# Optimization experiments

Hardware: AMD Instinct MI355X
Metric: run time of the kernel (lower is better)

The kernel has to match this reference:

```python
import jax, jax.numpy as jnp
import numpy as np

NX, NQ, NU, NY = 256, 64, 8, 4
N = 65536
EPS = 0.01
STD = 0.5


def setup_inputs() -> dict:
    key = jax.random.key(0)
    ks = jax.random.split(key, 8)
    return {
        "x": jax.random.normal(ks[0], (N, NX), jnp.float32),
        "u": jax.random.normal(ks[1], (N, NU), jnp.float32),
        "X": jax.random.normal(ks[2], (NX + NQ, NX + NQ), jnp.float32) * STD,
        "U": jax.random.normal(ks[3], (NX, NQ), jnp.float32) * STD,
        "Y1": jax.random.normal(ks[4], (NX, NX), jnp.float32) * STD,
        "XP": jax.random.normal(ks[5], (NX, NX), jnp.float32) * STD,
        "B2": jax.random.normal(ks[6], (NX, NU), jnp.float32) * STD,
        "D12": jax.random.normal(ks[7], (NQ, NU), jnp.float32) * STD,
        "bv": jnp.zeros((NQ,), jnp.float32),
        "t": 0,
    }


def _constrained(X, U, Y1, XP):
    # updateParameters(): build A, B1, C1, D11 from unconstrained params.
    P = XP @ XP.T + EPS * jnp.eye(NX, dtype=XP.dtype)
    H = X @ X.T + EPS * jnp.eye(NX + NQ, dtype=X.dtype)
    H11, H12, H22 = H[:NX, :NX], H[:NX, NX:], H[NX:, NX:]
    Y = -0.5 * (H11 + Y1 - Y1.T)
    Pinv = jnp.linalg.inv(P)
    A = Pinv @ Y                                   # [nx, nx]
    lam = 0.5 * jnp.diagonal(H22)                  # Lambda diagonal
    D11 = -jnp.tril(H22, -1) / lam[:, None]        # strictly lower triangular [nq, nq]
    C1 = U.T / lam[:, None]                        # [nq, nx]
    B1 = Pinv @ (-H12 - U)                         # [nx, nq]
    return A, B1, C1, D11


def _calc_w(base, D11):
    # Forward substitution: w_i = relu(base_i + sum_{j<i} D11[i,j] * w_j).
    # D11 is strictly lower triangular and unfilled w columns are zero, so a
    # full matvec against the carry is exact.
    nq = base.shape[1]

    def step(w, inp):
        i, row, b_col = inp                        # row: [nq], b_col: [Nbatch]
        wi = jax.nn.relu(b_col + w @ row)
        return w.at[:, i].set(wi), None

    w0 = jnp.zeros_like(base)
    w, _ = jax.lax.scan(step, w0, (jnp.arange(nq), D11, base.T))
    return w


def reference(x, u, X, U, Y1, XP, B2, D12, bv, t):
    A, B1, C1, D11 = _constrained(X, U, Y1, XP)
    base = x @ C1.T + u @ D12.T + bv               # [N, nq]
    w = _calc_w(base, D11)
    x_dot = x @ A.T + w @ B1.T + u @ B2.T          # [N, nx]
    return x_dot
```

## Files before the change

### kernel.cpp

```cpp
#include <hip/hip_runtime.h>

#define EPS_C 0.01f

typedef __attribute__((ext_vector_type(8))) short short8;
typedef __attribute__((ext_vector_type(4))) float f32x4;
typedef __attribute__((ext_vector_type(4))) unsigned short u16x4;
typedef __attribute__((ext_vector_type(8))) unsigned short u16x8;

#define WS_H    0
#define WS_C    102400
#define WS_C2   167936
#define WS_Y    233472
#define WS_RHS  299008
#define WS_D11  331776
#define WS_WFH  419840
#define WS_WFM  464896
#define WS_WFL  509952
#define WS_BBH  555008
#define WS_BBM  564224
#define WS_BBL  573440
#define WS_WG   582656
#define WS_E0   4776960
#define WS_E1   4781056

__device__ __forceinline__ int wfoff(int n, int k) {
    return (((n >> 4) * 44 + (k >> 5) * 4 + ((k >> 3) & 3)) << 7) + ((n & 15) << 3) + (k & 7);
}
__device__ __forceinline__ int bboff(int n, int k) {
    return (((n >> 4) * 36 + (k >> 5) * 4 + ((k >> 3) & 3)) << 7) + ((n & 15) << 3) + (k & 7);
}

__device__ __forceinline__ unsigned short f2bf(float f) {
    unsigned int u = __float_as_uint(f);
    unsigned int r = (u + 0x7fffu + ((u >> 16) & 1u)) >> 16;
    return (unsigned short)r;
}
__device__ __forceinline__ float bf2f(unsigned short h) {
    return __uint_as_float(((unsigned int)h) << 16);
}
__device__ __forceinline__ void split1(float f, unsigned short& h, unsigned short& m, unsigned short& l) {
    h = f2bf(f);
    float r1 = f - bf2f(h);
    m = f2bf(r1);
    l = f2bf(r1 - bf2f(m));
}
__device__ __forceinline__ void split8(const float* v, short8& h8, short8& m8, short8& l8) {
#pragma unroll
    for (int j = 0; j < 8; ++j) {
        unsigned short h, m, l;
        split1(v[j], h, m, l);
        h8[j] = (short)h; m8[j] = (short)m; l8[j] = (short)l;
    }
}

__global__ void k_build(const float* __restrict__ Xm, const float* __restrict__ XPm,
                        float* __restrict__ H, float* __restrict__ P) {
    int idx = blockIdx.x * 256 + threadIdx.x;
    if (idx < 102400) {
        int i = idx / 320, j = idx - i * 320;
        const float4* a = (const float4*)(Xm + i * 320);
        const float4* b = (const float4*)(Xm + j * 320);
        float s = 0.f;
        for (int k = 0; k < 80; ++k) {
            float4 va = a[k], vb = b[k];
            s += va.x * vb.x + va.y * vb.y + va.z * vb.z + va.w * vb.w;
        }
        H[idx] = (i == j) ? s + EPS_C : s;
    } else {
        idx -= 102400;
        if (idx < 65536) {
            int i = idx >> 8, j = idx & 255;
            const float4* a = (const float4*)(XPm + i * 256);
            const float4* b = (const float4*)(XPm + j * 256);
            float s = 0.f;
            for (int k = 0; k < 64; ++k) {
                float4 va = a[k], vb = b[k];
                s += va.x * vb.x + va.y * vb.y + va.z * vb.z + va.w * vb.w;
            }
            P[idx] = (i == j) ? s + EPS_C : s;
        }
    }
}

__global__ void k_derived(const float* __restrict__ H, const float* __restrict__ Um,
                          const float* __restrict__ Y1, const float* __restrict__ B2,
                          const float* __restrict__ D12,
                          float* __restrict__ Y, float* __restrict__ RHS,
                          float* __restrict__ D11g,
                          unsigned short* __restrict__ Bh, unsigned short* __restrict__ Bm,
                          unsigned short* __restrict__ Bl,
                          unsigned short* __restrict__ Bbh, unsigned short* __restrict__ Bbm,
                          unsigned short* __restrict__ Bbl) {
    int idx = blockIdx.x * 256 + threadIdx.x;
    if (idx < 65536) {
        int i = idx >> 8, j = idx & 255;
        Y[idx] = -0.5f * (H[i * 320 + j] + Y1[i * 256 + j] - Y1[j * 256 + i]);
        return;
    }
    idx -= 65536;
    if (idx < 16384) {
        RHS[idx] = -H[(idx >> 6) * 320 + 256 + (idx & 63)] - Um[idx];
        return;
    }
    idx -= 16384;
    if (idx < 4096) {
        int q = idx >> 6, j = idx & 63;
        float lam = 0.5f * H[(256 + q) * 320 + 256 + q];
        D11g[idx] = (j < q) ? -H[(256 + q) * 320 + 256 + j] / lam : 0.f;
        return;
    }
    idx -= 4096;
    if (idx < 8192) {
        int o = idx >> 5, cc = idx & 31;
        float f = (cc < 8) ? B2[o * 8 + cc] : 0.f;
        unsigned short h, m, l;
        split1(f, h, m, l);
        int off = wfoff(o, 256 + cc);
        Bh[off] = h; Bm[off] = m; Bl[off] = l;
        return;
    }
    idx -= 8192;
    if (idx < 18432) {
        int q = idx / 288, k = idx - q * 288;
        float f;
        if (k < 256) {
            float lam = 0.5f * H[(256 + q) * 320 + 256 + q];
            f = Um[(size_t)k * 64 + q] / lam;
        } else if (k < 264) f = D12[(size_t)q * 8 + (k - 256)];
        else f = 0.f;
        unsigned short h, m, l;
        split1(f, h, m, l);
        int off = bboff(q, k);
        Bbh[off] = h; Bbm[off] = m; Bbl[off] = l;
    }
}

__global__ void __launch_bounds__(256) k_inv8(const float* __restrict__ Cold, float* __restrict__ E, int b) {
    __shared__ __align__(16) float M[64 * 68];
    __shared__ __align__(16) float Rs[8 * 68];
    __shared__ __align__(16) float Ts[64 * 8];
    __shared__ float E8s[8 * 9];
    const int tid = threadIdx.x;
    const int ti = tid & 15, tj = tid >> 4;
#pragma unroll
    for (int t = 0; t < 4; ++t) {
        int e = tid + t * 256;
        int r = e >> 4, c4 = e & 15;
        float4 v = *(const float4*)&Cold[(size_t)(b * 64 + r) * 256 + b * 64 + c4 * 4];
        *(float4*)&M[r * 68 + c4 * 4] = v;
    }
    __syncthreads();
    for (int s = 0; s < 8; ++s) {
        if (tid < 64) {
            const int lane = tid;
            float e8[8];
#pragma unroll
            for (int j = 0; j < 8; ++j) e8[j] = 0.f;
            if (lane < 8) {
#pragma unroll
                for (int j = 0; j < 8; ++j) e8[j] = M[(s * 8 + lane) * 68 + s * 8 + j];
            }
#pragma unroll
            for (int k = 0; k < 8; ++k) {
                const float p = __shfl(e8[k], k);
                const float rinv = 1.0f / p;
                const float f = -e8[k] * rinv;
                const bool isk = (lane == k);
#pragma unroll
                for (int j = 0; j < 8; ++j) {
                    const float prj = __shfl(e8[j], k);
                    if (j == k) e8[j] = isk ? rinv : f;
                    else        e8[j] = isk ? prj * rinv : fmaf(f, prj, e8[j]);
                }
            }
            if (lane < 8) {
#pragma unroll
                for (int j = 0; j < 8; ++j) E8s[lane * 9 + j] = e8[j];
            }
        }
        __syncthreads();
#pragma unroll
        for (int t = 0; t < 2; ++t) {
            int e = tid + t * 256;
            int r = e >> 6, c = e & 63;
            Rs[r * 68 + c] = M[(s * 8 + r) * 68 + c];
        }
#pragma unroll
        for (int t = 0; t < 2; ++t) {
            int e = tid + t * 256;
            int i = e >> 3, c = e & 7;
            float acc = 0.f;
#pragma unroll
            for (int j = 0; j < 8; ++j) acc = fmaf(M[i * 68 + s * 8 + j], E8s[j * 9 + c], acc);
            Ts[i * 8 + c] = acc;
        }
        __syncthreads();
        {
            const bool rowIn = ((ti >> 1) == s);
            const bool colIn = ((tj >> 1) == s);
            const int i0 = ti * 4, j0 = tj * 4;
            float nv[4][4];
            if (rowIn && colIn) {
#pragma unroll
                for (int r = 0; r < 4; ++r)
#pragma unroll
                    for (int d = 0; d < 4; ++d)
                        nv[r][d] = E8s[(i0 - s * 8 + r) * 9 + (j0 - s * 8 + d)];
            } else if (rowIn) {
#pragma unroll
                for (int r = 0; r < 4; ++r)
#pragma unroll
                    for (int d = 0; d < 4; ++d) {
                        float acc = 0.f;
#pragma unroll
                        for (int c = 0; c < 8; ++c)
                            acc = fmaf(E8s[(i0 - s * 8 + r) * 9 + c], Rs[c * 68 + j0 + d], acc);
                        nv[r][d] = acc;
                    }
            } else if (colIn) {
#pragma unroll
                for (int r = 0; r < 4; ++r)
#pragma unroll
                    for (int d = 0; d < 4; ++d)
                        nv[r][d] = -Ts[(i0 + r) * 8 + (j0 - s * 8 + d)];
            } else {
#pragma unroll
                for (int r = 0; r < 4; ++r)
#pragma unroll
                    for (int d = 0; d < 4; ++d) {
                        float acc = M[(i0 + r) * 68 + j0 + d];
#pragma unroll
                        for (int c = 0; c < 8; ++c)
                            acc = fmaf(-Ts[(i0 + r) * 8 + c], Rs[c * 68 + j0 + d], acc);
                        nv[r][d] = acc;
                    }
            }
#pragma unroll
            for (int r = 0; r < 4; ++r)
#pragma unroll
                for (int d = 0; d < 4; ++d) M[(i0 + r) * 68 + j0 + d] = nv[r][d];
        }
        __syncthreads();
    }
#pragma unroll
    for (int t = 0; t < 4; ++t) {
        int e = tid + t * 256;
        int r = e >> 4, c4 = e & 15;
        float4 v = *(const float4*)&M[r * 68 + c4 * 4];
        *(float4*)&E[(size_t)r * 64 + c4 * 4] = v;
    }
}

__global__ void __launch_bounds__(256) k_gjS(const float* __restrict__ Cold, float* __restrict__ Cnew,
                                             const float* __restrict__ E, float* __restrict__ Eout,
                                             int b, int nb) {
    const int I = blockIdx.x >> 2, J = blockIdx.x & 3;
    const int tid = threadIdx.x;
    const int ti = tid & 15, tj = tid >> 4;
    if (I == b && J == b) {
        const int r = tid >> 2, seg = tid & 3;
#pragma unroll
        for (int t = 0; t < 4; ++t) {
            float4 v = *(const float4*)&E[(size_t)r * 64 + seg * 16 + t * 4];
            *(float4*)&Cnew[(size_t)(b * 64 + r) * 256 + b * 64 + seg * 16 + t * 4] = v;
        }
        return;
    }
    __shared__ __align__(16) float Es[64 * 68];
    __shared__ __align__(16) float S1[64 * 68];
    __shared__ __align__(16) float S2[64 * 68];
    for (int e = tid; e < 1024; e += 256) {
        int r = e >> 4, c4 = e & 15;
        float4 v = *(const float4*)&E[(size_t)r * 64 + c4 * 4];
        *(float4*)&Es[r * 68 + c4 * 4] = v;
    }
    if (I == b) {
        for (int e = tid; e < 1024; e += 256) {
            int r = e >> 4, c4 = e & 15;
            float4 v = *(const float4*)&Cold[(size_t)(b * 64 + r) * 256 + J * 64 + c4 * 4];
            *(float4*)&S1[r * 68 + c4 * 4] = v;
        }
        __syncthreads();
        float acc[4][4];
#pragma unroll
        for (int r = 0; r < 4; ++r)
#pragma unroll
            for (int d = 0; d < 4; ++d) acc[r][d] = 0.f;
        for (int mm = 0; mm < 64; ++mm) {
            float a4[4], b4[4];
#pragma unroll
            for (int d = 0; d < 4; ++d) { a4[d] = Es[(ti * 4 + d) * 68 + mm]; b4[d] = S1[mm * 68 + tj * 4 + d]; }
#pragma unroll
            for (int r = 0; r < 4; ++r)
#pragma unroll
                for (int d = 0; d < 4; ++d) acc[r][d] = fmaf(a4[r], b4[d], acc[r][d]);
        }
#pragma unroll
        for (int r = 0; r < 4; ++r) {
            float4 v = {acc[r][0], acc[r][1], acc[r][2], acc[r][3]};
            *(float4*)&Cnew[(size_t)(b * 64 + ti * 4 + r) * 256 + J * 64 + tj * 4] = v;
        }
        return;
    }
    if (J == b) {
        for (int e = tid; e < 1024; e += 256) {
            int r = e >> 4, c4 = e & 15;
            float4 v = *(const float4*)&Cold[(size_t)(I * 64 + r) * 256 + b * 64 + c4 * 4];
            *(float4*)&S1[r * 68 + c4 * 4] = v;
        }
        __syncthreads();
        float acc[4][4];
#pragma unroll
        for (int r = 0; r < 4; ++r)
#pragma unroll
            for (int d = 0; d < 4; ++d) acc[r][d] = 0.f;
        for (int kk = 0; kk < 64; ++kk) {
            float a4[4], b4[4];
#pragma unroll
            for (int d = 0; d < 4; ++d) { a4[d] = S1[(ti * 4 + d) * 68 + kk]; b4[d] = Es[kk * 68 + tj * 4 + d]; }
#pragma unroll
            for (int r = 0; r < 4; ++r)
#pragma unroll
                for (int d = 0; d < 4; ++d) acc[r][d] = fmaf(a4[r], b4[d], acc[r][d]);
        }
#pragma unroll
        for (int r = 0; r < 4; ++r) {
            float4 v = {-acc[r][0], -acc[r][1], -acc[r][2], -acc[r][3]};
            *(float4*)&Cnew[(size_t)(I * 64 + ti * 4 + r) * 256 + b * 64 + tj * 4] = v;
        }
        return;
    }
    for (int e = tid; e < 1024; e += 256) {
        int r = e >> 4, c4 = e & 15;
        float4 v = *(const float4*)&Cold[(size_t)(I * 64 + r) * 256 + b * 64 + c4 * 4];
        *(float4*)&S1[r * 68 + c4 * 4] = v;
        float4 w = *(const float4*)&Cold[(size_t)(b * 64 + r) * 256 + J * 64 + c4 * 4];
        *(float4*)&S2[r * 68 + c4 * 4] = w;
    }
    __syncthreads();
    float t4[4][4];
#pragma unroll
    for (int r = 0; r < 4; ++r)
#pragma unroll
        for (int d = 0; d < 4; ++d) t4[r][d] = 0.f;
    for (int kk = 0; kk < 64; ++kk) {
        float a4[4], b4[4];
#pragma unroll
        for (int d = 0; d < 4; ++d) { a4[d] = S1[(ti * 4 + d) * 68 + kk]; b4[d] = Es[kk * 68 + tj * 4 + d]; }
#pragma unroll
        for (int r = 0; r < 4; ++r)
#pragma unroll
            for (int d = 0; d < 4; ++d) t4[r][d] = fmaf(a4[r], b4[d], t4[r][d]);
    }
    __syncthreads();
#pragma unroll
    for (int r = 0; r < 4; ++r)
#pragma unroll
        for (int d = 0; d < 4; ++d) S1[(ti * 4 + r) * 68 + tj * 4 + d] = t4[r][d];
    __syncthreads();
    float acc[4][4];
#pragma unroll
    for (int r = 0; r < 4; ++r) {
        float4 cv = *(const float4*)&Cold[(size_t)(I * 64 + ti * 4 + r) * 256 + J * 64 + tj * 4];
        acc[r][0] = cv.x; acc[r][1] = cv.y; acc[r][2] = cv.z; acc[r][3] = cv.w;
    }
    for (int kk = 0; kk < 64; ++kk) {
        float a4[4], b4[4];
#pragma unroll
        for (int d = 0; d < 4; ++d) { a4[d] = S1[(ti * 4 + d) * 68 + kk]; b4[d] = S2[kk * 68 + tj * 4 + d]; }
#pragma unroll
        for (int r = 0; r < 4; ++r)
#pragma unroll
            for (int d = 0; d < 4; ++d) acc[r][d] = fmaf(-a4[r], b4[d], acc[r][d]);
    }
#pragma unroll
    for (int r = 0; r < 4; ++r) {
        float4 v = {acc[r][0], acc[r][1], acc[r][2], acc[r][3]};
        *(float4*)&Cnew[(size_t)(I * 64 + ti * 4 + r) * 256 + J * 64 + tj * 4] = v;
    }
    if (I == nb && J == nb) {
        float* M   = Es;
        float* Rs2 = S2;
        float* Ts2 = S2 + 1024;
        float* E8s = S2 + 1664;
        __syncthreads();
#pragma unroll
        for (int r = 0; r < 4; ++r)
#pragma unroll
            for (int d = 0; d < 4; ++d)
                M[(ti * 4 + r) * 68 + tj * 4 + d] = acc[r][d];
        __syncthreads();
        for (int s = 0; s < 8; ++s) {
            if (tid < 64) {
                const int lane = tid;
                float e8[8];
#pragma unroll
                for (int j = 0; j < 8; ++j) e8[j] = 0.f;
                if (lane < 8) {
#pragma unroll
                    for (int j = 0; j < 8; ++j) e8[j] = M[(s * 8 + lane) * 68 + s * 8 + j];
                }
#pragma unroll
                for (int k = 0; k < 8; ++k) {
                    const float p = __shfl(e8[k], k);
                    const float rinv = 1.0f / p;
                    const float f = -e8[k] * rinv;
                    const bool isk = (lane == k);
#pragma unroll
                    for (int j = 0; j < 8; ++j) {
                        const float prj = __shfl(e8[j], k);
                        if (j == k) e8[j] = isk ? rinv : f;
                        else        e8[j] = isk ? prj * rinv : fmaf(f, prj, e8[j]);
                    }
                }
                if (lane < 8) {
#pragma unroll
                    for (int j = 0; j < 8; ++j) E8s[lane * 9 + j] = e8[j];
                }
            }
            __syncthreads();
#pragma unroll
            for (int t = 0; t < 2; ++t) {
                int e = tid + t * 256;
                int r = e >> 6, c = e & 63;
                Rs2[r * 68 + c] = M[(s * 8 + r) * 68 + c];
            }
#pragma unroll
            for (int t = 0; t < 2; ++t) {
                int e = tid + t * 256;
                int i = e >> 3, c = e & 7;
                float a2 = 0.f;
#pragma unroll
                for (int j = 0; j < 8; ++j) a2 = fmaf(M[i * 68 + s * 8 + j], E8s[j * 9 + c], a2);
                Ts2[i * 8 + c] = a2;
            }
            __syncthreads();
            {
                const bool rowIn = ((ti >> 1) == s);
                const bool colIn = ((tj >> 1) == s);
                const int i0 = ti * 4, j0 = tj * 4;
                float nv[4][4];
                if (rowIn && colIn) {
#pragma unroll
                    for (int r = 0; r < 4; ++r)
#pragma unroll
                        for (int d = 0; d < 4; ++d)
                            nv[r][d] = E8s[(i0 - s * 8 + r) * 9 + (j0 - s * 8 + d)];
                } else if (rowIn) {
#pragma unroll
                    for (int r = 0; r < 4; ++r)
#pragma unroll
                        for (int d = 0; d < 4; ++d) {
                            float a2 = 0.f;
#pragma unroll
                            for (int c = 0; c < 8; ++c)
                                a2 = fmaf(E8s[(i0 - s * 8 + r) * 9 + c], Rs2[c * 68 + j0 + d], a2);
                            nv[r][d] = a2;
                        }
                } else if (colIn) {
#pragma unroll
                    for (int r = 0; r < 4; ++r)
#pragma unroll
                        for (int d = 0; d < 4; ++d)
                            nv[r][d] = -Ts2[(i0 + r) * 8 + (j0 - s * 8 + d)];
                } else {
#pragma unroll
                    for (int r = 0; r < 4; ++r)
#pragma unroll
                        for (int d = 0; d < 4; ++d) {
                            float a2 = M[(i0 + r) * 68 + j0 + d];
#pragma unroll
                            for (int c = 0; c < 8; ++c)
                                a2 = fmaf(-Ts2[(i0 + r) * 8 + c], Rs2[c * 68 + j0 + d], a2);
                            nv[r][d] = a2;
                        }
                }
#pragma unroll
                for (int r = 0; r < 4; ++r)
#pragma unroll
                    for (int d = 0; d < 4; ++d) M[(i0 + r) * 68 + j0 + d] = nv[r][d];
            }
            __syncthreads();
        }
#pragma unroll
        for (int t = 0; t < 4; ++t) {
            int e = tid + t * 256;
            int r = e >> 4, c4 = e & 15;
            float4 v = *(const float4*)&M[r * 68 + c4 * 4];
            *(float4*)&Eout[(size_t)r * 64 + c4 * 4] = v;
        }
    }
}

__global__ void __launch_bounds__(256) k_apply2(const float* __restrict__ PI, const float* __restrict__ Y,
                                                const float* __restrict__ RHS,
                                                unsigned short* __restrict__ Bh, unsigned short* __restrict__ Bm,
                                                unsigned short* __restrict__ Bl) {
    const int i0 = ((int)blockIdx.x / 5) * 64;
    const int c0 = ((int)blockIdx.x % 5) * 64;
    __shared__ __align__(16) float S1[64 * 68], S2[64 * 68];
    const int tid = threadIdx.x;
    const int ti = tid & 15, tj = tid >> 4;
    float acc[4][4];
#pragma unroll
    for (int r = 0; r < 4; ++r)
#pragma unroll
        for (int d = 0; d < 4; ++d) acc[r][d] = 0.f;
    for (int kc = 0; kc < 4; ++kc) {
        __syncthreads();
        for (int e = tid; e < 1024; e += 256) {
            int i = e >> 4, k4 = e & 15;
            float4 v = *(const float4*)&PI[(size_t)(i0 + i) * 256 + kc * 64 + k4 * 4];
            S1[(k4 * 4 + 0) * 68 + i] = v.x;
            S1[(k4 * 4 + 1) * 68 + i] = v.y;
            S1[(k4 * 4 + 2) * 68 + i] = v.z;
            S1[(k4 * 4 + 3) * 68 + i] = v.w;
            float4 w;
            if (c0 < 256) w = *(const float4*)&Y[(size_t)(kc * 64 + i) * 256 + c0 + k4 * 4];
            else          w = *(const float4*)&RHS[(size_t)(kc * 64 + i) * 64 + k4 * 4];
            *(float4*)&S2[i * 68 + k4 * 4] = w;
        }
        __syncthreads();
        for (int kk = 0; kk < 64; ++kk) {
            float4 pv = *(const float4*)&S1[kk * 68 + ti * 4];
            float4 gv = *(const float4*)&S2[kk * 68 + tj * 4];
            float p4[4] = {pv.x, pv.y, pv.z, pv.w};
            float g4[4] = {gv.x, gv.y, gv.z, gv.w};
#pragma unroll
            for (int r = 0; r < 4; ++r)
#pragma unroll
                for (int d = 0; d < 4; ++d) acc[r][d] = fmaf(p4[r], g4[d], acc[r][d]);
        }
    }
    const int pc0 = (c0 < 256) ? c0 : 288;
#pragma unroll
    for (int r = 0; r < 4; ++r)
#pragma unroll
        for (int d = 0; d < 4; ++d) {
            unsigned short h, m, l;
            split1(acc[r][d], h, m, l);
            int off = wfoff(i0 + ti * 4 + r, pc0 + tj * 4 + d);
            Bh[off] = h; Bm[off] = m; Bl[off] = l;
        }
}

#define XSTR 264
__global__ void __launch_bounds__(256, 3) k_base(const float* __restrict__ x, const float* __restrict__ u,
                                                 const unsigned short* __restrict__ Bbh,
                                                 const unsigned short* __restrict__ Bbm,
                                                 const unsigned short* __restrict__ Bbl,
                                                 const float* __restrict__ bv,
                                                 float* __restrict__ wg) {
    __shared__ __align__(16) unsigned short Ah[32 * XSTR];
    __shared__ __align__(16) unsigned short Am[32 * XSTR];
    __shared__ __align__(16) unsigned short Al[32 * XSTR];
    const int tid = threadIdx.x;
    const int r0 = blockIdx.x * 32;
    {
        const float4* xg4 = (const float4*)(x + (size_t)r0 * 256);
#pragma unroll
        for (int i = 0; i < 8; ++i) {
            int e = tid + i * 256, r = e >> 6, c4 = e & 63;
            float4 v = xg4[e];
            float vv[4] = {v.x, v.y, v.z, v.w};
            u16x4 hv, mv, lv;
#pragma unroll
            for (int j = 0; j < 4; ++j) {
                unsigned short h, m, l;
                split1(vv[j], h, m, l);
                hv[j] = h; mv[j] = m; lv[j] = l;
            }
            *(u16x4*)&Ah[r * XSTR + c4 * 4] = hv;
            *(u16x4*)&Am[r * XSTR + c4 * 4] = mv;
            *(u16x4*)&Al[r * XSTR + c4 * 4] = lv;
        }
    }
    __syncthreads();
    const int lane = tid & 63, wid = tid >> 6;
    const int n0 = wid * 16;
    const int lr = lane & 15, lg = lane >> 4;
    const int lk = lg * 8;
    const int fb = wid * 4608 + lg * 128 + lr * 8;
    f32x4 acc[2];
    acc[0] = (f32x4){0.f, 0.f, 0.f, 0.f};
    acc[1] = (f32x4){0.f, 0.f, 0.f, 0.f};
    for (int kt = 0; kt < 9; ++kt) {
        const int ka = kt * 32 + lk;
        short8 a_h[2], a_m[2], a_l[2];
        if (kt < 8) {
            a_h[0] = *(const short8*)&Ah[lr * XSTR + ka];
            a_h[1] = *(const short8*)&Ah[(16 + lr) * XSTR + ka];
            a_m[0] = *(const short8*)&Am[lr * XSTR + ka];
            a_m[1] = *(const short8*)&Am[(16 + lr) * XSTR + ka];
            a_l[0] = *(const short8*)&Al[lr * XSTR + ka];
            a_l[1] = *(const short8*)&Al[(16 + lr) * XSTR + ka];
        } else {
            if (lg == 0) {
                float vv[8];
                const float4* up = (const float4*)&u[(size_t)(r0 + lr) * 8];
                float4 v0 = up[0], v1 = up[1];
                vv[0] = v0.x; vv[1] = v0.y; vv[2] = v0.z; vv[3] = v0.w;
                vv[4] = v1.x; vv[5] = v1.y; vv[6] = v1.z; vv[7] = v1.w;
                split8(vv, a_h[0], a_m[0], a_l[0]);
                const float4* up2 = (const float4*)&u[(size_t)(r0 + 16 + lr) * 8];
                float4 w0 = up2[0], w1 = up2[1];
                vv[0] = w0.x; vv[1] = w0.y; vv[2] = w0.z; vv[3] = w0.w;
                vv[4] = w1.x; vv[5] = w1.y; vv[6] = w1.z; vv[7] = w1.w;
                split8(vv, a_h[1], a_m[1], a_l[1]);
            } else {
                short8 z = {0, 0, 0, 0, 0, 0, 0, 0};
                a_h[0] = z; a_h[1] = z; a_m[0] = z; a_m[1] = z; a_l[0] = z; a_l[1] = z;
            }
        }
        const int off = fb + kt * 512;
        short8 b_h = *(const short8*)&Bbh[off];
        short8 b_m = *(const short8*)&Bbm[off];
        short8 b_l = *(const short8*)&Bbl[off];
#pragma unroll
        for (int m = 0; m < 2; ++m) {
            acc[m] = __builtin_amdgcn_mfma_f32_16x16x32_bf16(a_h[m], b_h, acc[m], 0, 0, 0);
            acc[m] = __builtin_amdgcn_mfma_f32_16x16x32_bf16(a_m[m], b_h, acc[m], 0, 0, 0);
            acc[m] = __builtin_amdgcn_mfma_f32_16x16x32_bf16(a_h[m], b_m, acc[m], 0, 0, 0);
            acc[m] = __builtin_amdgcn_mfma_f32_16x16x32_bf16(a_l[m], b_h, acc[m], 0, 0, 0);
            acc[m] = __builtin_amdgcn_mfma_f32_16x16x32_bf16(a_m[m], b_m, acc[m], 0, 0, 0);
            acc[m] = __builtin_amdgcn_mfma_f32_16x16x32_bf16(a_h[m], b_l, acc[m], 0, 0, 0);
        }
    }
    const float bvv = bv[n0 + lr];
#pragma unroll
    for (int m = 0; m < 2; ++m)
#pragma unroll
        for (int j = 0; j < 4; ++j)
            wg[(size_t)(r0 + m * 16 + lg * 4 + j) * 64 + n0 + lr] = acc[m][j] + bvv;
}

__global__ void __launch_bounds__(256) k_rec(float* __restrict__ wg, const float* __restrict__ D11g) {
    __shared__ float D[64 * 64];
    const int tid = threadIdx.x;
#pragma unroll
    for (int t = 0; t < 16; ++t) D[tid + t * 256] = D11g[tid + t * 256];
    __syncthreads();
    const size_t r = (size_t)blockIdx.x * 256 + tid;
    float w[64];
    float* wr = wg + r * 64;
#pragma unroll
    for (int c = 0; c < 16; ++c) {
        float4 v = *(const float4*)&wr[c * 4];
        w[4 * c] = v.x; w[4 * c + 1] = v.y; w[4 * c + 2] = v.z; w[4 * c + 3] = v.w;
    }
    w[0] = fmaxf(w[0], 0.f);
#pragma unroll
    for (int i = 1; i < 64; ++i) {
        float s0 = w[i], s1 = 0.f, s2 = 0.f, s3 = 0.f;
#pragma unroll
        for (int j = 0; j + 3 < i; j += 4) {
            s0 = fmaf(w[j + 0], D[i * 64 + j + 0], s0);
            s1 = fmaf(w[j + 1], D[i * 64 + j + 1], s1);
            s2 = fmaf(w[j + 2], D[i * 64 + j + 2], s2);
            s3 = fmaf(w[j + 3], D[i * 64 + j + 3], s3);
        }
#pragma unroll
        for (int j = i & ~3; j < i; ++j) s0 = fmaf(w[j], D[i * 64 + j], s0);
        w[i] = fmaxf((s0 + s1) + (s2 + s3), 0.f);
    }
#pragma unroll
    for (int c = 0; c < 16; ++c) {
        float4 v = {w[4 * c], w[4 * c + 1], w[4 * c + 2], w[4 * c + 3]};
        *(float4*)&wr[c * 4] = v;
    }
}

__global__ void __launch_bounds__(256, 3) k_m2(const float* __restrict__ x, const float* __restrict__ wg,
                                               const float* __restrict__ u,
                                               const unsigned short* __restrict__ Bh,
                                               const unsigned short* __restrict__ Bm,
                                               const unsigned short* __restrict__ Bl,
                                               float* __restrict__ out) {
    __shared__ __align__(16) unsigned short Ah[32 * XSTR];
    __shared__ __align__(16) unsigned short Am[32 * XSTR];
    __shared__ __align__(16) unsigned short Al[32 * XSTR];
    const int tid = threadIdx.x;
    const int r0 = blockIdx.x * 32;
    {
        const float4* xg4 = (const float4*)(x + (size_t)r0 * 256);
#pragma unroll
        for (int i = 0; i < 8; ++i) {
            int e = tid + i * 256, r = e >> 6, c4 = e & 63;
            float4 v = xg4[e];
            float vv[4] = {v.x, v.y, v.z, v.w};
            u16x4 hv, mv, lv;
#pragma unroll
            for (int j = 0; j < 4; ++j) {
                unsigned short h, m, l;
                split1(vv[j], h, m, l);
                hv[j] = h; mv[j] = m; lv[j] = l;
            }
            *(u16x4*)&Ah[r * XSTR + c4 * 4] = hv;
            *(u16x4*)&Am[r * XSTR + c4 * 4] = mv;
            *(u16x4*)&Al[r * XSTR + c4 * 4] = lv;
        }
    }
    __syncthreads();
    const int lane = tid & 63, wid = tid >> 6;
    const int n0 = wid * 64;
    const int lr = lane & 15, lg = lane >> 4;
    const int lk = lg * 8;
    const int lgoff = lg * 128 + lr * 8;
    int fb[4];
#pragma unroll
    for (int nf = 0; nf < 4; ++nf) fb[nf] = (wid * 4 + nf) * 5632 + lgoff;
    f32x4 acc[2][4];
#pragma unroll
    for (int m = 0; m < 2; ++m)
#pragma unroll
        for (int nf = 0; nf < 4; ++nf) acc[m][nf] = (f32x4){0.f, 0.f, 0.f, 0.f};

#define M2_MFMA6()                                                                               \
    for (int nf = 0; nf < 4; ++nf) {                                                             \
        for (int m = 0; m < 2; ++m) {                                                            \
            acc[m][nf] = __builtin_amdgcn_mfma_f32_16x16x32_bf16(a_h[m], b_h[nf], acc[m][nf], 0, 0, 0); \
            acc[m][nf] = __builtin_amdgcn_mfma_f32_16x16x32_bf16(a_m[m], b_h[nf], acc[m][nf], 0, 0, 0); \
            acc[m][nf] = __builtin_amdgcn_mfma_f32_16x16x32_bf16(a_h[m], b_m[nf], acc[m][nf], 0, 0, 0); \
            acc[m][nf] = __builtin_amdgcn_mfma_f32_16x16x32_bf16(a_l[m], b_h[nf], acc[m][nf], 0, 0, 0); \
            acc[m][nf] = __builtin_amdgcn_mfma_f32_16x16x32_bf16(a_m[m], b_m[nf], acc[m][nf], 0, 0, 0); \
            acc[m][nf] = __builtin_amdgcn_mfma_f32_16x16x32_bf16(a_h[m], b_l[nf], acc[m][nf], 0, 0, 0); \
        }                                                                                        \
    }

    for (int kt = 0; kt < 8; ++kt) {
        const int ka = kt * 32 + lk;
        short8 a_h[2], a_m[2], a_l[2];
        a_h[0] = *(const short8*)&Ah[lr * XSTR + ka];
        a_h[1] = *(const short8*)&Ah[(16 + lr) * XSTR + ka];
        a_m[0] = *(const short8*)&Am[lr * XSTR + ka];
        a_m[1] = *(const short8*)&Am[(16 + lr) * XSTR + ka];
        a_l[0] = *(const short8*)&Al[lr * XSTR + ka];
        a_l[1] = *(const short8*)&Al[(16 + lr) * XSTR + ka];
        short8 b_h[4], b_m[4], b_l[4];
#pragma unroll
        for (int nf = 0; nf < 4; ++nf) {
            const int off = fb[nf] + kt * 512;
            b_h[nf] = *(const short8*)&Bh[off];
            b_m[nf] = *(const short8*)&Bm[off];
            b_l[nf] = *(const short8*)&Bl[off];
        }
#pragma unroll
        M2_MFMA6()
    }
    {
        short8 a_h[2], a_m[2], a_l[2];
        if (lg == 0) {
            float vv[8];
            const float4* up = (const float4*)&u[(size_t)(r0 + lr) * 8];
            float4 v0 = up[0], v1 = up[1];
            vv[0] = v0.x; vv[1] = v0.y; vv[2] = v0.z; vv[3] = v0.w;
            vv[4] = v1.x; vv[5] = v1.y; vv[6] = v1.z; vv[7] = v1.w;
            split8(vv, a_h[0], a_m[0], a_l[0]);
            const float4* up2 = (const float4*)&u[(size_t)(r0 + 16 + lr) * 8];
            float4 w0 = up2[0], w1 = up2[1];
            vv[0] = w0.x; vv[1] = w0.y; vv[2] = w0.z; vv[3] = w0.w;
            vv[4] = w1.x; vv[5] = w1.y; vv[6] = w1.z; vv[7] = w1.w;
            split8(vv, a_h[1], a_m[1], a_l[1]);
        } else {
            short8 z = {0, 0, 0, 0, 0, 0, 0, 0};
            a_h[0] = z; a_h[1] = z; a_m[0] = z; a_m[1] = z; a_l[0] = z; a_l[1] = z;
        }
        short8 b_h[4], b_m[4], b_l[4];
#pragma unroll
        for (int nf = 0; nf < 4; ++nf) {
            const int off = fb[nf] + 8 * 512;
            b_h[nf] = *(const short8*)&Bh[off];
            b_m[nf] = *(const short8*)&Bm[off];
            b_l[nf] = *(const short8*)&Bl[off];
        }
#pragma unroll
        M2_MFMA6()
    }
    for (int kt = 9; kt < 11; ++kt) {
        const int wc = (kt - 9) * 32 + lk;
        short8 a_h[2], a_m[2], a_l[2];
        {
            float vv[8];
            const float4* wp = (const float4*)&wg[(size_t)(r0 + lr) * 64 + wc];
            float4 v0 = wp[0], v1 = wp[1];
            vv[0] = v0.x; vv[1] = v0.y; vv[2] = v0.z; vv[3] = v0.w;
            vv[4] = v1.x; vv[5] = v1.y; vv[6] = v1.z; vv[7] = v1.w;
            split8(vv, a_h[0], a_m[0], a_l[0]);
            const float4* wp2 = (const float4*)&wg[(size_t)(r0 + 16 + lr) * 64 + wc];
            float4 w0 = wp2[0], w1 = wp2[1];
            vv[0] = w0.x; vv[1] = w0.y; vv[2] = w0.z; vv[3] = w0.w;
            vv[4] = w1.x; vv[5] = w1.y; vv[6] = w1.z; vv[7] = w1.w;
            split8(vv, a_h[1], a_m[1], a_l[1]);
        }
        short8 b_h[4], b_m[4], b_l[4];
#pragma unroll
        for (int nf = 0; nf < 4; ++nf) {
            const int off = fb[nf] + kt * 512;
            b_h[nf] = *(const short8*)&Bh[off];
            b_m[nf] = *(const short8*)&Bm[off];
            b_l[nf] = *(const short8*)&Bl[off];
        }
#pragma unroll
        for (int nf = 0; nf < 4; ++nf) {
#pragma unroll
            for (int m = 0; m < 2; ++m) {
                acc[m][nf] = __builtin_amdgcn_mfma_f32_16x16x32_bf16(a_h[m], b_h[nf], acc[m][nf], 0, 0, 0);
                acc[m][nf] = __builtin_amdgcn_mfma_f32_16x16x32_bf16(a_m[m], b_h[nf], acc[m][nf], 0, 0, 0);
                acc[m][nf] = __builtin_amdgcn_mfma_f32_16x16x32_bf16(a_h[m], b_m[nf], acc[m][nf], 0, 0, 0);
                acc[m][nf] = __builtin_amdgcn_mfma_f32_16x16x32_bf16(a_l[m], b_h[nf], acc[m][nf], 0, 0, 0);
                acc[m][nf] = __builtin_amdgcn_mfma_f32_16x16x32_bf16(a_m[m], b_m[nf], acc[m][nf], 0, 0, 0);
                acc[m][nf] = __builtin_amdgcn_mfma_f32_16x16x32_bf16(a_h[m], b_l[nf], acc[m][nf], 0, 0, 0);
                acc[m][nf] = __builtin_amdgcn_mfma_f32_16x16x32_bf16(a_m[m], b_l[nf], acc[m][nf], 0, 0, 0);
                acc[m][nf] = __builtin_amdgcn_mfma_f32_16x16x32_bf16(a_l[m], b_m[nf], acc[m][nf], 0, 0, 0);
            }
        }
    }
#pragma unroll
    for (int m = 0; m < 2; ++m)
#pragma unroll
        for (int nf = 0; nf < 4; ++nf)
#pragma unroll
            for (int j = 0; j < 4; ++j)
                out[(size_t)(r0 + m * 16 + lg * 4 + j) * 256 + n0 + nf * 16 + lr] = acc[m][nf][j];
}

extern "C" void kernel_launch(void* const* d_in, const int* in_sizes, int n_in,
                              void* d_out, int out_size, void* d_ws, size_t ws_size,
                              hipStream_t stream) {
    const float* x   = (const float*)d_in[0];
    const float* u   = (const float*)d_in[1];
    const float* Xm  = (const float*)d_in[2];
    const float* Um  = (const float*)d_in[3];
    const float* Y1  = (const float*)d_in[4];
    const float* XPm = (const float*)d_in[5];
    const float* B2  = (const float*)d_in[6];
    const float* D12 = (const float*)d_in[7];
    const float* bv  = (const float*)d_in[8];
    float* out = (float*)d_out;
    float* ws  = (float*)d_ws;

    float* H    = ws + WS_H;
    float* C0   = ws + WS_C;
    float* C1   = ws + WS_C2;
    float* Y    = ws + WS_Y;
    float* RHS  = ws + WS_RHS;
    float* D11g = ws + WS_D11;
    float* E0   = ws + WS_E0;
    float* E1   = ws + WS_E1;
    unsigned short* Bh  = (unsigned short*)(ws + WS_WFH);
    unsigned short* Bm  = (unsigned short*)(ws + WS_WFM);
    unsigned short* Bl  = (unsigned short*)(ws + WS_WFL);
    unsigned short* Bbh = (unsigned short*)(ws + WS_BBH);
    unsigned short* Bbm = (unsigned short*)(ws + WS_BBM);
    unsigned short* Bbl = (unsigned short*)(ws + WS_BBL);
    float* wg = ws + WS_WG;

    k_build<<<656, 256, 0, stream>>>(Xm, XPm, H, C0);
    k_derived<<<441, 256, 0, stream>>>(H, Um, Y1, B2, D12, Y, RHS, D11g,
                                       Bh, Bm, Bl, Bbh, Bbm, Bbl);
    k_base<<<2048, 256, 0, stream>>>(x, u, Bbh, Bbm, Bbl, bv, wg);
    k_rec<<<256, 256, 0, stream>>>(wg, D11g);
    k_inv8<<<1, 256, 0, stream>>>(C0, E0, 0);
    k_gjS<<<16, 256, 0, stream>>>(C0, C1, E0, E1, 0, 1);
    k_gjS<<<16, 256, 0, stream>>>(C1, C0, E1, E0, 1, 2);
    k_gjS<<<16, 256, 0, stream>>>(C0, C1, E0, E1, 2, 3);
    k_gjS<<<16, 256, 0, stream>>>(C1, C0, E1, E0, 3, -1);
    k_apply2<<<20, 256, 0, stream>>>(C0, Y, RHS, Bh, Bm, Bl);
    k_m2<<<2048, 256, 0, stream>>>(x, wg, u, Bh, Bm, Bl, out);
}
```

Before: 340.7 us.

## Fuse recurrence into base GEMM and merge first block inverse into derived kernel

```diff
diff --git a/kernel.cpp b/kernel.cpp
--- a/kernel.cpp
+++ b/kernel.cpp
@@ -82,7 +82,7 @@
     }
 }
 
-__global__ void k_derived(const float* __restrict__ H, const float* __restrict__ Um,
+__global__ void __launch_bounds__(256) k_derived(const float* __restrict__ H, const float* __restrict__ Um,
                           const float* __restrict__ Y1, const float* __restrict__ B2,
                           const float* __restrict__ D12,
                           float* __restrict__ Y, float* __restrict__ RHS,
@@ -90,8 +90,125 @@
                           unsigned short* __restrict__ Bh, unsigned short* __restrict__ Bm,
                           unsigned short* __restrict__ Bl,
                           unsigned short* __restrict__ Bbh, unsigned short* __restrict__ Bbm,
-                          unsigned short* __restrict__ Bbl) {
-    int idx = blockIdx.x * 256 + threadIdx.x;
+                          unsigned short* __restrict__ Bbl,
+                          const float* __restrict__ C0, float* __restrict__ E0) {
+    __shared__ __align__(16) float M[64 * 68];
+    __shared__ __align__(16) float Rs[8 * 68];
+    __shared__ __align__(16) float Ts[64 * 8];
+    __shared__ float E8s[8 * 9];
+    const int tid = threadIdx.x;
+    if (blockIdx.x == 441) {
+        const int ti = tid & 15, tj = tid >> 4;
+#pragma unroll
+        for (int t = 0; t < 4; ++t) {
+            int e = tid + t * 256;
+            int r = e >> 4, c4 = e & 15;
+            float4 v = *(const float4*)&C0[(size_t)r * 256 + c4 * 4];
+            *(float4*)&M[r * 68 + c4 * 4] = v;
+        }
+        __syncthreads();
+        for (int s = 0; s < 8; ++s) {
+            if (tid < 64) {
+                const int lane = tid;
+                float e8[8];
+#pragma unroll
+                for (int j = 0; j < 8; ++j) e8[j] = 0.f;
+                if (lane < 8) {
+#pragma unroll
+                    for (int j = 0; j < 8; ++j) e8[j] = M[(s * 8 + lane) * 68 + s * 8 + j];
+                }
+#pragma unroll
+                for (int k = 0; k < 8; ++k) {
+                    const float p = __shfl(e8[k], k);
+                    const float rinv = 1.0f / p;
+                    const float f = -e8[k] * rinv;
+                    const bool isk = (lane == k);
+#pragma unroll
+                    for (int j = 0; j < 8; ++j) {
+                        const float prj = __shfl(e8[j], k);
+                        if (j == k) e8[j] = isk ? rinv : f;
+                        else        e8[j] = isk ? prj * rinv : fmaf(f, prj, e8[j]);
+                    }
+                }
+                if (lane < 8) {
+#pragma unroll
+                    for (int j = 0; j < 8; ++j) E8s[lane * 9 + j] = e8[j];
+                }
+            }
+            __syncthreads();
+#pragma unroll
+            for (int t = 0; t < 2; ++t) {
+                int e = tid + t * 256;
+                int r = e >> 6, c = e & 63;
+                Rs[r * 68 + c] = M[(s * 8 + r) * 68 + c];
+            }
+#pragma unroll
+            for (int t = 0; t < 2; ++t) {
+                int e = tid + t * 256;
+                int i = e >> 3, c = e & 7;
+                float acc = 0.f;
+#pragma unroll
+                for (int j = 0; j < 8; ++j) acc = fmaf(M[i * 68 + s * 8 + j], E8s[j * 9 + c], acc);
+                Ts[i * 8 + c] = acc;
+            }
+            __syncthreads();
+            {
+                const bool rowIn = ((ti >> 1) == s);
+                const bool colIn = ((tj >> 1) == s);
+                const int i0 = ti * 4, j0 = tj * 4;
+                float nv[4][4];
+                if (rowIn && colIn) {
+#pragma unroll
+                    for (int r = 0; r < 4; ++r)
+#pragma unroll
+                        for (int d = 0; d < 4; ++d)
+                            nv[r][d] = E8s[(i0 - s * 8 + r) * 9 + (j0 - s * 8 + d)];
+                } else if (rowIn) {
+#pragma unroll
+                    for (int r = 0; r < 4; ++r)
+#pragma unroll
+                        for (int d = 0; d < 4; ++d) {
+                            float acc = 0.f;
+#pragma unroll
+                            for (int c = 0; c < 8; ++c)
+                                acc = fmaf(E8s[(i0 - s * 8 + r) * 9 + c], Rs[c * 68 + j0 + d], acc);
+                            nv[r][d] = acc;
+                        }
+                } else if (colIn) {
+#pragma unroll
+                    for (int r = 0; r < 4; ++r)
+#pragma unroll
+                        for (int d = 0; d < 4; ++d)
+                            nv[r][d] = -Ts[(i0 + r) * 8 + (j0 - s * 8 + d)];
+                } else {
+#pragma unroll
+                    for (int r = 0; r < 4; ++r)
+#pragma unroll
+                        for (int d = 0; d < 4; ++d) {
+                            float acc = M[(i0 + r) * 68 + j0 + d];
+#pragma unroll
+                            for (int c = 0; c < 8; ++c)
+                                acc = fmaf(-Ts[(i0 + r) * 8 + c], Rs[c * 68 + j0 + d], acc);
+                            nv[r][d] = acc;
+                        }
+                }
+#pragma unroll
+                for (int r = 0; r < 4; ++r)
+#pragma unroll
+                    for (int d = 0; d < 4; ++d) M[(i0 + r) * 68 + j0 + d] = nv[r][d];
+            }
+            __syncthreads();
+        }
+#pragma unroll
+        for (int t = 0; t < 4; ++t) {
+            int e = tid + t * 256;
+            int r = e >> 4, c4 = e & 15;
+            float4 v = *(const float4*)&M[r * 68 + c4 * 4];
+            *(float4*)&E0[(size_t)r * 64 + c4 * 4] = v;
+        }
+        return;
+    }
+    int idx = blockIdx.x * 256 + tid;
     if (idx < 65536) {
         int i = idx >> 8, j = idx & 255;
         Y[idx] = -0.5f * (H[i * 320 + j] + Y1[i * 256 + j] - Y1[j * 256 + i]);
@@ -132,122 +249,6 @@
         split1(f, h, m, l);
         int off = bboff(q, k);
         Bbh[off] = h; Bbm[off] = m; Bbl[off] = l;
-    }
-}
-
-__global__ void __launch_bounds__(256) k_inv8(const float* __restrict__ Cold, float* __restrict__ E, int b) {
-    __shared__ __align__(16) float M[64 * 68];
-    __shared__ __align__(16) float Rs[8 * 68];
-    __shared__ __align__(16) float Ts[64 * 8];
-    __shared__ float E8s[8 * 9];
-    const int tid = threadIdx.x;
-    const int ti = tid & 15, tj = tid >> 4;
-#pragma unroll
-    for (int t = 0; t < 4; ++t) {
-        int e = tid + t * 256;
-        int r = e >> 4, c4 = e & 15;
-        float4 v = *(const float4*)&Cold[(size_t)(b * 64 + r) * 256 + b * 64 + c4 * 4];
-        *(float4*)&M[r * 68 + c4 * 4] = v;
-    }
-    __syncthreads();
-    for (int s = 0; s < 8; ++s) {
-        if (tid < 64) {
-            const int lane = tid;
-            float e8[8];
-#pragma unroll
-            for (int j = 0; j < 8; ++j) e8[j] = 0.f;
-            if (lane < 8) {
-#pragma unroll
-                for (int j = 0; j < 8; ++j) e8[j] = M[(s * 8 + lane) * 68 + s * 8 + j];
-            }
-#pragma unroll
-            for (int k = 0; k < 8; ++k) {
-                const float p = __shfl(e8[k], k);
-                const float rinv = 1.0f / p;
-                const float f = -e8[k] * rinv;
-                const bool isk = (lane == k);
-#pragma unroll
-                for (int j = 0; j < 8; ++j) {
-                    const float prj = __shfl(e8[j], k);
-                    if (j == k) e8[j] = isk ? rinv : f;
-                    else        e8[j] = isk ? prj * rinv : fmaf(f, prj, e8[j]);
-                }
-            }
-            if (lane < 8) {
-#pragma unroll
-                for (int j = 0; j < 8; ++j) E8s[lane * 9 + j] = e8[j];
-            }
-        }
-        __syncthreads();
-#pragma unroll
-        for (int t = 0; t < 2; ++t) {
-            int e = tid + t * 256;
-            int r = e >> 6, c = e & 63;
-            Rs[r * 68 + c] = M[(s * 8 + r) * 68 + c];
-        }
-#pragma unroll
-        for (int t = 0; t < 2; ++t) {
-            int e = tid + t * 256;
-            int i = e >> 3, c = e & 7;
-            float acc = 0.f;
-#pragma unroll
-            for (int j = 0; j < 8; ++j) acc = fmaf(M[i * 68 + s * 8 + j], E8s[j * 9 + c], acc);
-            Ts[i * 8 + c] = acc;
-        }
-        __syncthreads();
-        {
-            const bool rowIn = ((ti >> 1) == s);
-            const bool colIn = ((tj >> 1) == s);
-            const int i0 = ti * 4, j0 = tj * 4;
-            float nv[4][4];
-            if (rowIn && colIn) {
-#pragma unroll
-                for (int r = 0; r < 4; ++r)
-#pragma unroll
-                    for (int d = 0; d < 4; ++d)
-                        nv[r][d] = E8s[(i0 - s * 8 + r) * 9 + (j0 - s * 8 + d)];
-            } else if (rowIn) {
-#pragma unroll
-                for (int r = 0; r < 4; ++r)
-#pragma unroll
-                    for (int d = 0; d < 4; ++d) {
-                        float acc = 0.f;
-#pragma unroll
-                        for (int c = 0; c < 8; ++c)
-                            acc = fmaf(E8s[(i0 - s * 8 + r) * 9 + c], Rs[c * 68 + j0 + d], acc);
-                        nv[r][d] = acc;
-                    }
-            } else if (colIn) {
-#pragma unroll
-                for (int r = 0; r < 4; ++r)
-#pragma unroll
-                    for (int d = 0; d < 4; ++d)
-                        nv[r][d] = -Ts[(i0 + r) * 8 + (j0 - s * 8 + d)];
-            } else {
-#pragma unroll
-                for (int r = 0; r < 4; ++r)
-#pragma unroll
-                    for (int d = 0; d < 4; ++d) {
-                        float acc = M[(i0 + r) * 68 + j0 + d];
-#pragma unroll
-                        for (int c = 0; c < 8; ++c)
-                            acc = fmaf(-Ts[(i0 + r) * 8 + c], Rs[c * 68 + j0 + d], acc);
-                        nv[r][d] = acc;
-                    }
-            }
-#pragma unroll
-            for (int r = 0; r < 4; ++r)
-#pragma unroll
-                for (int d = 0; d < 4; ++d) M[(i0 + r) * 68 + j0 + d] = nv[r][d];
-        }
-        __syncthreads();
-    }
-#pragma unroll
-    for (int t = 0; t < 4; ++t) {
-        int e = tid + t * 256;
-        int r = e >> 4, c4 = e & 15;
-        float4 v = *(const float4*)&M[r * 68 + c4 * 4];
-        *(float4*)&E[(size_t)r * 64 + c4 * 4] = v;
     }
 }
 
@@ -545,15 +546,18 @@
 }
 
 #define XSTR 264
-__global__ void __launch_bounds__(256, 3) k_base(const float* __restrict__ x, const float* __restrict__ u,
-                                                 const unsigned short* __restrict__ Bbh,
-                                                 const unsigned short* __restrict__ Bbm,
-                                                 const unsigned short* __restrict__ Bbl,
-                                                 const float* __restrict__ bv,
-                                                 float* __restrict__ wg) {
+__global__ void __launch_bounds__(256, 2) k_basrec(const float* __restrict__ x, const float* __restrict__ u,
+                                                   const unsigned short* __restrict__ Bbh,
+                                                   const unsigned short* __restrict__ Bbm,
+                                                   const unsigned short* __restrict__ Bbl,
+                                                   const float* __restrict__ bv,
+                                                   const float* __restrict__ D11g,
+                                                   float* __restrict__ wg) {
     __shared__ __align__(16) unsigned short Ah[32 * XSTR];
     __shared__ __align__(16) unsigned short Am[32 * XSTR];
     __shared__ __align__(16) unsigned short Al[32 * XSTR];
+    __shared__ float bs[32 * 65];
+    __shared__ float Ds[64 * 64];
     const int tid = threadIdx.x;
     const int r0 = blockIdx.x * 32;
     {
@@ -574,6 +578,8 @@
             *(u16x4*)&Am[r * XSTR + c4 * 4] = mv;
             *(u16x4*)&Al[r * XSTR + c4 * 4] = lv;
         }
+#pragma unroll
+        for (int t = 0; t < 16; ++t) Ds[tid + t * 256] = D11g[tid + t * 256];
     }
     __syncthreads();
     const int lane = tid & 63, wid = tid >> 6;
@@ -626,47 +632,40 @@
             acc[m] = __builtin_amdgcn_mfma_f32_16x16x32_bf16(a_h[m], b_l, acc[m], 0, 0, 0);
         }
     }
-    const float bvv = bv[n0 + lr];
-#pragma unroll
-    for (int m = 0; m < 2; ++m)
-#pragma unroll
-        for (int j = 0; j < 4; ++j)
-            wg[(size_t)(r0 + m * 16 + lg * 4 + j) * 64 + n0 + lr] = acc[m][j] + bvv;
-}
-
-__global__ void __launch_bounds__(256) k_rec(float* __restrict__ wg, const float* __restrict__ D11g) {
-    __shared__ float D[64 * 64];
-    const int tid = threadIdx.x;
-#pragma unroll
-    for (int t = 0; t < 16; ++t) D[tid + t * 256] = D11g[tid + t * 256];
+    {
+        const float bvv = bv[n0 + lr];
+#pragma unroll
+        for (int m = 0; m < 2; ++m)
+#pragma unroll
+            for (int j = 0; j < 4; ++j)
+                bs[(m * 16 + lg * 4 + j) * 65 + n0 + lr] = acc[m][j] + bvv;
+    }
     __syncthreads();
-    const size_t r = (size_t)blockIdx.x * 256 + tid;
-    float w[64];
-    float* wr = wg + r * 64;
-#pragma unroll
-    for (int c = 0; c < 16; ++c) {
-        float4 v = *(const float4*)&wr[c * 4];
-        w[4 * c] = v.x; w[4 * c + 1] = v.y; w[4 * c + 2] = v.z; w[4 * c + 3] = v.w;
-    }
-    w[0] = fmaxf(w[0], 0.f);
-#pragma unroll
-    for (int i = 1; i < 64; ++i) {
-        float s0 = w[i], s1 = 0.f, s2 = 0.f, s3 = 0.f;
-#pragma unroll
-        for (int j = 0; j + 3 < i; j += 4) {
-            s0 = fmaf(w[j + 0], D[i * 64 + j + 0], s0);
-            s1 = fmaf(w[j + 1], D[i * 64 + j + 1], s1);
-            s2 = fmaf(w[j + 2], D[i * 64 + j + 2], s2);
-            s3 = fmaf(w[j + 3], D[i * 64 + j + 3], s3);
-        }
-#pragma unroll
-        for (int j = i & ~3; j < i; ++j) s0 = fmaf(w[j], D[i * 64 + j], s0);
-        w[i] = fmaxf((s0 + s1) + (s2 + s3), 0.f);
-    }
-#pragma unroll
-    for (int c = 0; c < 16; ++c) {
-        float4 v = {w[4 * c], w[4 * c + 1], w[4 * c + 2], w[4 * c + 3]};
-        *(float4*)&wr[c * 4] = v;
+    if (tid < 32) {
+        float w[64];
+#pragma unroll
+        for (int c = 0; c < 64; ++c) w[c] = bs[tid * 65 + c];
+        w[0] = fmaxf(w[0], 0.f);
+#pragma unroll
+        for (int i = 1; i < 64; ++i) {
+            float s0 = w[i], s1 = 0.f, s2 = 0.f, s3 = 0.f;
+#pragma unroll
+            for (int j = 0; j + 3 < i; j += 4) {
+                s0 = fmaf(w[j + 0], Ds[i * 64 + j + 0], s0);
+                s1 = fmaf(w[j + 1], Ds[i * 64 + j + 1], s1);
+                s2 = fmaf(w[j + 2], Ds[i * 64 + j + 2], s2);
+                s3 = fmaf(w[j + 3], Ds[i * 64 + j + 3], s3);
+            }
+#pragma unroll
+            for (int j = i & ~3; j < i; ++j) s0 = fmaf(w[j], Ds[i * 64 + j], s0);
+            w[i] = fmaxf((s0 + s1) + (s2 + s3), 0.f);
+        }
+        float* wr = wg + (size_t)(r0 + tid) * 64;
+#pragma unroll
+        for (int c = 0; c < 16; ++c) {
+            float4 v = {w[4 * c], w[4 * c + 1], w[4 * c + 2], w[4 * c + 3]};
+            *(float4*)&wr[c * 4] = v;
+        }
     }
 }
 
@@ -856,11 +855,9 @@
     float* wg = ws + WS_WG;
 
     k_build<<<656, 256, 0, stream>>>(Xm, XPm, H, C0);
-    k_derived<<<441, 256, 0, stream>>>(H, Um, Y1, B2, D12, Y, RHS, D11g,
-                                       Bh, Bm, Bl, Bbh, Bbm, Bbl);
-    k_base<<<2048, 256, 0, stream>>>(x, u, Bbh, Bbm, Bbl, bv, wg);
-    k_rec<<<256, 256, 0, stream>>>(wg, D11g);
-    k_inv8<<<1, 256, 0, stream>>>(C0, E0, 0);
+    k_derived<<<442, 256, 0, stream>>>(H, Um, Y1, B2, D12, Y, RHS, D11g,
+                                       Bh, Bm, Bl, Bbh, Bbm, Bbl, C0, E0);
+    k_basrec<<<2048, 256, 0, stream>>>(x, u, Bbh, Bbm, Bbl, bv, D11g, wg);
     k_gjS<<<16, 256, 0, stream>>>(C0, C1, E0, E1, 0, 1);
     k_gjS<<<16, 256, 0, stream>>>(C1, C0, E1, E0, 1, 2);
     k_gjS<<<16, 256, 0, stream>>>(C0, C1, E0, E1, 2, 3);
```

New measurement: 363.0 us. 1.07x slower.
